# Optimization experiments

Measured on AMD Instinct MI355X. Metric: run time of the kernel, lower is better.

The kernel has to match this reference:

```python
import jax, jax.numpy as jnp
import numpy as np

EMBED_DIM = 1024
NUM_HEADS = 16
HEAD_DIM = EMBED_DIM // NUM_HEADS
FF_DIM = 4096
LN_EPS = 1e-5


def layer_norm(x, scale, bias):
    mu = jnp.mean(x, axis=-1, keepdims=True)
    var = jnp.mean(jnp.square(x - mu), axis=-1, keepdims=True)
    return (x - mu) * jax.lax.rsqrt(var + LN_EPS) * scale + bias


def setup_inputs() -> dict:
    key = jax.random.key(0)
    ks = jax.random.split(key, 9)
    E, F = EMBED_DIM, FF_DIM
    s = lambda d: 1.0 / np.sqrt(d)
    return {
        "x": jax.random.normal(ks[0], (2, 2048, E), dtype=jnp.float32),
        "qkv_w": jax.random.uniform(ks[1], (3 * E, E), jnp.float32, -s(E), s(E)),
        "out_w": jax.random.uniform(ks[2], (E, E), jnp.float32, -s(E), s(E)),
        "ff_up_w": jax.random.uniform(ks[3], (F, E), jnp.float32, -s(E), s(E)),
        "ff_down_w": jax.random.uniform(ks[4], (E, F), jnp.float32, -s(F), s(F)),
        "norm1_scale": jnp.ones((E,), jnp.float32),
        "norm1_bias": jnp.zeros((E,), jnp.float32),
        "norm2_scale": jnp.ones((E,), jnp.float32),
        "norm2_bias": jnp.zeros((E,), jnp.float32),
    }


def reference(x, qkv_w, out_w, ff_up_w, ff_down_w,
              norm1_scale, norm1_bias, norm2_scale, norm2_bias):
    B, S, E = x.shape
    H, D = NUM_HEADS, HEAD_DIM

    # --- attention sublayer ---
    residual = x
    h = layer_norm(x, norm1_scale, norm1_bias)
    qkv = h @ qkv_w.T                               # [B,S,3E]
    qkv = qkv.reshape(B, S, 3, H, D).transpose(2, 0, 3, 1, 4)  # [3,B,H,S,D]
    q, k, v = qkv[0], qkv[1], qkv[2]
    scores = jnp.einsum("bhqd,bhkd->bhqk", q, k) / np.sqrt(D)
    probs = jax.nn.softmax(scores, axis=-1)
    attn = jnp.einsum("bhqk,bhkd->bhqd", probs, v)  # [B,H,S,D]
    attn = attn.transpose(0, 2, 1, 3).reshape(B, S, E)
    x = residual + attn @ out_w.T

    # --- FFN sublayer ---
    residual = x
    h = layer_norm(x, norm2_scale, norm2_bias)
    h = jax.nn.gelu(h @ ff_up_w.T, approximate=False)
    h = h @ ff_down_w.T
    return residual + h
```

## Files before the change

kernel.cpp:

```cpp
#include <hip/hip_runtime.h>

typedef unsigned short u16;
typedef unsigned int u32;
typedef __attribute__((ext_vector_type(8))) short bf16x8;
typedef __attribute__((ext_vector_type(4))) float f32x4;

#define MFMA_BF16(a, b, c) __builtin_amdgcn_mfma_f32_16x16x32_bf16((a), (b), (c), 0, 0, 0)
#define BAR() __builtin_amdgcn_s_barrier()
#define WAITV(n) asm volatile("s_waitcnt vmcnt(" #n ")" ::: "memory")

#if __has_builtin(__builtin_amdgcn_exp2f)
#define EXP2(x) __builtin_amdgcn_exp2f(x)
#else
#define EXP2(x) exp2f(x)
#endif

__device__ __forceinline__ u16 f2bf(float f) {
    u32 u = __builtin_bit_cast(u32, f);
    u32 r = u + 0x7FFFu + ((u >> 16) & 1u);
    return (u16)(r >> 16);
}

__device__ __forceinline__ void gld16(const void* g, void* s) {
    __builtin_amdgcn_global_load_lds(
        (const __attribute__((address_space(1))) unsigned int*)g,
        (__attribute__((address_space(3))) unsigned int*)s, 16, 0, 0);
}

__global__ __launch_bounds__(256) void cvtall_k(const float* __restrict__ w0,
                                                const float* __restrict__ w1,
                                                const float* __restrict__ w2,
                                                const float* __restrict__ w3,
                                                u16* o0, u16* o1, u16* o2, u16* o3) {
    int j = blockIdx.x * 256 + threadIdx.x;
    const float* src; u16* dst;
    if (j < 786432)                       { src = w0; dst = o0; }
    else if ((j -= 786432) < 262144)      { src = w1; dst = o1; }
    else if ((j -= 262144) < 1048576)     { src = w2; dst = o2; }
    else { j -= 1048576;                    src = w3; dst = o3; }
    float4 v = ((const float4*)src)[j];
    ushort4 o;
    o.x = f2bf(v.x); o.y = f2bf(v.y); o.z = f2bf(v.z); o.w = f2bf(v.w);
    ((ushort4*)dst)[j] = o;
}

__global__ __launch_bounds__(256) void ln_k(const float* __restrict__ x,
                                            u16* __restrict__ out,
                                            const float* __restrict__ sc,
                                            const float* __restrict__ bi) {
    const int row = blockIdx.x;
    const int tid = threadIdx.x;
    const float4 v = ((const float4*)(x + (size_t)row * 1024))[tid];
    float s  = v.x + v.y + v.z + v.w;
    float s2 = v.x*v.x + v.y*v.y + v.z*v.z + v.w*v.w;
    #pragma unroll
    for (int m = 32; m; m >>= 1) { s += __shfl_xor(s, m); s2 += __shfl_xor(s2, m); }
    __shared__ float red[8];
    const int w = tid >> 6, l = tid & 63;
    if (l == 0) { red[w] = s; red[4 + w] = s2; }
    __syncthreads();
    s  = red[0] + red[1] + red[2] + red[3];
    s2 = red[4] + red[5] + red[6] + red[7];
    const float mu  = s * (1.0f / 1024.0f);
    const float var = s2 * (1.0f / 1024.0f) - mu * mu;
    const float rs  = rsqrtf(var + 1e-5f);
    const float4 sv = ((const float4*)sc)[tid];
    const float4 bv = ((const float4*)bi)[tid];
    ushort4 o;
    o.x = f2bf((v.x - mu) * rs * sv.x + bv.x);
    o.y = f2bf((v.y - mu) * rs * sv.y + bv.y);
    o.z = f2bf((v.z - mu) * rs * sv.z + bv.z);
    o.w = f2bf((v.w - mu) * rs * sv.w + bv.w);
    ((ushort4*)(out + (size_t)row * 1024))[tid] = o;
}

template<int NT, int EPI>
__global__ __launch_bounds__(512, 1) void gemm256_k(const u16* __restrict__ A,
                                                    const u16* __restrict__ B,
                                                    u16* __restrict__ Cb,
                                                    u16* __restrict__ vtout,
                                                    int M, int N, int K) {
    extern __shared__ u16 L[];
    const int tid = threadIdx.x;
    const int w = tid >> 6, l = tid & 63, g = l >> 4, lc = l & 15;
    const int wr = w >> 2, wc = w & 3;

    const int gx = gridDim.x, gy = gridDim.y;
    const int lin = blockIdx.x + gx * blockIdx.y;
    const int rx = gx >> 2, cy = gy >> 1;
    const int xcd = lin & 7, slot = lin >> 3;
    const int brow = (xcd & 3) * rx + (slot % rx);
    const int bcol = (xcd >> 2) * cy + (slot / rx);
    const int row0 = brow * 256, col0 = bcol * 256;

    const u16* gA = A + (size_t)row0 * K;
    const u16* gB = B + (size_t)col0 * K;
    int srow[4], soct[4];
    #pragma unroll
    for (int p = 0; p < 4; ++p) {
        const int idx = p * 512 + tid;
        srow[p] = idx >> 3;
        soct[p] = (idx & 7) ^ (srow[p] & 7);
    }

#define STG(t, p) do { \
        char* base_ = (char*)L + ((t) & 1) * 65536; \
        gld16(gA + (size_t)srow[p] * K + (size_t)(t) * 64 + soct[p] * 8, \
              base_ + ((p) * 512 + tid) * 16); \
        gld16(gB + (size_t)srow[p] * K + (size_t)(t) * 64 + soct[p] * 8, \
              base_ + 32768 + ((p) * 512 + tid) * 16); \
    } while (0)

    f32x4 acc[8][4] = {};

    STG(0, 0); STG(0, 1); STG(0, 2); STG(0, 3);

    const int ocx = lc & 7;

    for (int t = 0; t < NT; ++t) {
        const bool pf = (t + 1 < NT);
        if (pf) { STG(t + 1, 0); WAITV(2); } else { WAITV(0); }
        BAR();

        const u16* La = L + (t & 1) * 32768;
        const u16* Lb = La + 16384;

        bf16x8 bfr[4][2];
        #pragma unroll
        for (int j = 0; j < 4; ++j)
            #pragma unroll
            for (int kk = 0; kk < 2; ++kk)
                bfr[j][kk] = *(const bf16x8*)
                    &Lb[(wc * 64 + j * 16 + lc) * 64 + (((kk * 4 + g) ^ ocx) * 8)];

        #pragma unroll
        for (int ph = 0; ph < 4; ++ph) {
            if (ph == 2) BAR();
            bf16x8 af[2][2];
            #pragma unroll
            for (int ii = 0; ii < 2; ++ii)
                #pragma unroll
                for (int kk = 0; kk < 2; ++kk)
                    af[ii][kk] = *(const bf16x8*)
                        &La[(wr * 128 + (ph * 2 + ii) * 16 + lc) * 64 +
                            (((kk * 4 + g) ^ ocx) * 8)];
            __builtin_amdgcn_s_setprio(1);
            #pragma unroll
            for (int ii = 0; ii < 2; ++ii)
                #pragma unroll
                for (int j = 0; j < 4; ++j)
                    #pragma unroll
                    for (int kk = 0; kk < 2; ++kk)
                        acc[ph * 2 + ii][j] = MFMA_BF16(af[ii][kk], bfr[j][kk],
                                                        acc[ph * 2 + ii][j]);
            __builtin_amdgcn_s_setprio(0);
            if (pf && ph < 3) STG(t + 1, ph + 1);
        }
    }
#undef STG

    #pragma unroll
    for (int i = 0; i < 8; ++i)
        #pragma unroll
        for (int j = 0; j < 4; ++j) {
            const int rowb = row0 + wr * 128 + i * 16 + g * 4;
            const int col  = col0 + wc * 64 + j * 16 + lc;
            if (EPI == 0 && col >= 2048) {
                u32 lo, hi;
                asm("v_cvt_pk_bf16_f32 %0, %1, %2"
                    : "=v"(lo) : "v"(acc[i][j][0]), "v"(acc[i][j][1]));
                asm("v_cvt_pk_bf16_f32 %0, %1, %2"
                    : "=v"(hi) : "v"(acc[i][j][2]), "v"(acc[i][j][3]));
                const int hd = col - 2048, bb = rowb >> 11, token = rowb & 2047;
                uint2 pk; pk.x = lo; pk.y = hi;
                *(uint2*)(vtout + ((size_t)(bb * 16 + (hd >> 6)) * 64 + (hd & 63)) * 2048
                          + token) = pk;
            } else {
                #pragma unroll
                for (int r = 0; r < 4; ++r) {
                    const size_t off = (size_t)(rowb + r) * N + col;
                    const float v = acc[i][j][r];
                    if (EPI == 0) {
                        const float vv = (col < 1024) ? v * 0.180336880f : v;
                        Cb[off] = f2bf(vv);
                    } else {
                        const float gv = 0.5f * v * (1.0f + erff(v * 0.70710678118f));
                        Cb[off] = f2bf(gv);
                    }
                }
            }
        }
}

template<int NT>
__global__ __launch_bounds__(512, 1) void gemm128w8_k(const u16* __restrict__ A,
                                                      const u16* __restrict__ B,
                                                      float* __restrict__ Cf,
                                                      const float* __restrict__ resid,
                                                      int M, int N, int K) {
    extern __shared__ u16 L[];
    const int tid = threadIdx.x;
    const int w = tid >> 6, l = tid & 63, g = l >> 4, lc = l & 15;
    const int wr = w >> 1, wc = w & 1;
    const int row0 = blockIdx.x * 128, col0 = blockIdx.y * 128;

    const u16* gA = A + (size_t)row0 * K;
    const u16* gB = B + (size_t)col0 * K;
    const int srow = tid >> 3;
    const int soct = (tid & 7) ^ (srow & 7);

#define STG8(t, p) do { \
        const u16* src_ = ((p) < 2) ? gB : gA; \
        const int row_ = (((p) & 1) << 6) + srow; \
        gld16(src_ + (size_t)row_ * K + (size_t)(t) * 64 + soct * 8, \
              (char*)L + ((t) & 1) * 32768 + (p) * 8192 + tid * 16); \
    } while (0)

    f32x4 acc[2][4] = {};

    STG8(0, 0); STG8(0, 1); STG8(0, 2); STG8(0, 3);

    const int ocx = lc & 7;

    for (int t = 0; t < NT; ++t) {
        const bool pf = (t + 1 < NT);
        if (pf) { STG8(t + 1, 0); WAITV(1); } else { WAITV(0); }
        BAR();

        const u16* Lb = L + (t & 1) * 16384;
        const u16* La = Lb + 8192;

        bf16x8 bfr[4][2];
        #pragma unroll
        for (int j = 0; j < 4; ++j)
            #pragma unroll
            for (int kk = 0; kk < 2; ++kk)
                bfr[j][kk] = *(const bf16x8*)
                    &Lb[(wc * 64 + j * 16 + lc) * 64 + (((kk * 4 + g) ^ ocx) * 8)];

        {
            bf16x8 af[2];
            #pragma unroll
            for (int kk = 0; kk < 2; ++kk)
                af[kk] = *(const bf16x8*)
                    &La[(wr * 32 + lc) * 64 + (((kk * 4 + g) ^ ocx) * 8)];
            __builtin_amdgcn_s_setprio(1);
            #pragma unroll
            for (int j = 0; j < 4; ++j)
                #pragma unroll
                for (int kk = 0; kk < 2; ++kk)
                    acc[0][j] = MFMA_BF16(af[kk], bfr[j][kk], acc[0][j]);
            __builtin_amdgcn_s_setprio(0);
        }
        if (pf) { STG8(t + 1, 1); STG8(t + 1, 2); }
        BAR();
        {
            bf16x8 af[2];
            #pragma unroll
            for (int kk = 0; kk < 2; ++kk)
                af[kk] = *(const bf16x8*)
                    &La[(wr * 32 + 16 + lc) * 64 + (((kk * 4 + g) ^ ocx) * 8)];
            __builtin_amdgcn_s_setprio(1);
            #pragma unroll
            for (int j = 0; j < 4; ++j)
                #pragma unroll
                for (int kk = 0; kk < 2; ++kk)
                    acc[1][j] = MFMA_BF16(af[kk], bfr[j][kk], acc[1][j]);
            __builtin_amdgcn_s_setprio(0);
        }
        if (pf) STG8(t + 1, 3);
    }
#undef STG8

    #pragma unroll
    for (int i = 0; i < 2; ++i)
        #pragma unroll
        for (int j = 0; j < 4; ++j)
            #pragma unroll
            for (int r = 0; r < 4; ++r) {
                const int row = row0 + wr * 32 + i * 16 + g * 4 + r;
                const int col = col0 + wc * 64 + j * 16 + lc;
                const size_t off = (size_t)row * N + col;
                Cf[off] = acc[i][j][r] + resid[off];
            }
}

__global__ __launch_bounds__(512) void attn_k(const u16* __restrict__ qkv,
                                              const u16* __restrict__ vt,
                                              u16* __restrict__ ctx) {
    const int bh = blockIdx.x;
    const int qt = blockIdx.y;
    const int b = bh >> 4, h = bh & 15;
    const int tid = threadIdx.x, w = tid >> 6, l = tid & 63, g = l >> 4, lc = l & 15;
    const size_t tok0 = (size_t)b * 2048;

    const u16* Qg  = qkv + (tok0 + qt * 128) * 3072 + h * 64;
    const u16* Kg  = qkv + tok0 * 3072 + 1024 + h * 64;
    const u16* Vtg = vt + (size_t)bh * 64 * 2048;

    __shared__ u16 Ks[2][64 * 64];
    __shared__ u16 Vts[2][64 * 64];
    __shared__ u16 QPs[128 * 64];
    u16* Pw = QPs + w * 1024;

    {
        const int q0r = tid >> 3,         q0c = (tid & 7) ^ (q0r & 7);
        const int q1r = (tid + 512) >> 3, q1c = ((tid + 512) & 7) ^ (q1r & 7);
        gld16(Qg + (size_t)q0r * 3072 + q0c * 8, (char*)QPs + tid * 16);
        gld16(Qg + (size_t)q1r * 3072 + q1c * 8, (char*)QPs + (tid + 512) * 16);
    }
    const int skr = tid >> 3, skc = (tid & 7) ^ (skr & 7);
    const u16* kp = Kg + (size_t)skr * 3072 + skc * 8;
    const u16* vp = Vtg + (size_t)skr * 2048 + skc * 8;
    gld16(kp, (char*)Ks[0] + tid * 16);
    gld16(vp, (char*)Vts[0] + tid * 16);
    kp += 64 * 3072; vp += 64;
    __syncthreads();

    bf16x8 qf[2];
    {
        const int qrow = w * 16 + lc;
        qf[0] = *(const bf16x8*)&QPs[qrow * 64 + ((g       ^ (lc & 7)) * 8)];
        qf[1] = *(const bf16x8*)&QPs[qrow * 64 + (((4 + g) ^ (lc & 7)) * 8)];
    }

    f32x4 oacc[4] = {};
    float mrow = -1e30f, lrow = 0.0f;
    const int hsw = (lc & 7) << 3;

    for (int kt = 0; kt < 32; ++kt) {
        WAITV(0);
        BAR();
        if (kt + 1 < 32) {
            gld16(kp, (char*)Ks[(kt + 1) & 1] + tid * 16);
            gld16(vp, (char*)Vts[(kt + 1) & 1] + tid * 16);
            kp += 64 * 3072; vp += 64;
        }
        const u16* Kc = Ks[kt & 1];
        const u16* Vc = Vts[kt & 1];

        f32x4 sacc[4] = {};
        __builtin_amdgcn_s_setprio(1);
        #pragma unroll
        for (int kk = 0; kk < 2; ++kk)
            #pragma unroll
            for (int nt = 0; nt < 4; ++nt) {
                const int krow = nt * 16 + lc;
                const bf16x8 kb = *(const bf16x8*)
                    &Kc[krow * 64 + (((kk * 4 + g) ^ (lc & 7)) * 8)];
                sacc[nt] = MFMA_BF16(kb, qf[kk], sacc[nt]);
            }
        __builtin_amdgcn_s_setprio(0);

        float mx;
        {
            const float* sv = (const float*)sacc;
            float m = sv[0];
            #pragma unroll
            for (int q = 0; q < 7; ++q) {
                float t;
                asm("v_max3_f32 %0, %1, %2, %3"
                    : "=v"(t) : "v"(m), "v"(sv[2 * q + 1]), "v"(sv[2 * q + 2]));
                m = t;
            }
            mx = fmaxf(m, sv[15]);
        }
        mx = fmaxf(mx, __shfl_xor(mx, 16));
        mx = fmaxf(mx, __shfl_xor(mx, 32));
        const bool ru = __any(mx > mrow + 8.0f);
        float corr = 1.0f;
        if (ru) {
            const float mnew = fmaxf(mrow, mx);
            corr = EXP2(mrow - mnew);
            mrow = mnew;
        }

        float p[4][4];
        float ps = 0.0f;
        #pragma unroll
        for (int nt = 0; nt < 4; ++nt)
            #pragma unroll
            for (int r = 0; r < 4; ++r) {
                const float pv = EXP2(sacc[nt][r] - mrow);
                p[nt][r] = pv;
                ps += pv;
            }
        ps += __shfl_xor(ps, 16);
        ps += __shfl_xor(ps, 32);

        #pragma unroll
        for (int nt = 0; nt < 4; ++nt) {
            uint2 pk;
            asm("v_cvt_pk_bf16_f32 %0, %1, %2" : "=v"(pk.x) : "v"(p[nt][0]), "v"(p[nt][1]));
            asm("v_cvt_pk_bf16_f32 %0, %1, %2" : "=v"(pk.y) : "v"(p[nt][2]), "v"(p[nt][3]));
            *(uint2*)&Pw[lc * 64 + ((nt * 16 + g * 4) ^ hsw)] = pk;
        }

        if (ru) {
            lrow = lrow * corr + ps;
            float cq[4];
            #pragma unroll
            for (int r = 0; r < 4; ++r) cq[r] = __shfl(corr, g * 4 + r);
            #pragma unroll
            for (int nt = 0; nt < 4; ++nt)
                #pragma unroll
                for (int r = 0; r < 4; ++r) oacc[nt][r] *= cq[r];
        } else {
            lrow += ps;
        }

        __builtin_amdgcn_s_setprio(1);
        #pragma unroll
        for (int kk = 0; kk < 2; ++kk) {
            const bf16x8 pa = *(const bf16x8*)
                &Pw[lc * 64 + ((kk * 32 + g * 8) ^ hsw)];
            #pragma unroll
            for (int nt = 0; nt < 4; ++nt) {
                const int vrow = nt * 16 + lc;
                const bf16x8 vb = *(const bf16x8*)
                    &Vc[vrow * 64 + (((kk * 4 + g) ^ (lc & 7)) * 8)];
                oacc[nt] = MFMA_BF16(pa, vb, oacc[nt]);
            }
        }
        __builtin_amdgcn_s_setprio(0);
    }

    float lq[4];
    #pragma unroll
    for (int r = 0; r < 4; ++r) lq[r] = 1.0f / __shfl(lrow, g * 4 + r);
    #pragma unroll
    for (int nt = 0; nt < 4; ++nt)
        #pragma unroll
        for (int r = 0; r < 4; ++r) {
            const float o = oacc[nt][r] * lq[r];
            const size_t token = tok0 + qt * 128 + w * 16 + g * 4 + r;
            ctx[token * 1024 + h * 64 + nt * 16 + lc] = f2bf(o);
        }
}

extern "C" void kernel_launch(void* const* d_in, const int* in_sizes, int n_in,
                              void* d_out, int out_size, void* d_ws, size_t ws_size,
                              hipStream_t stream) {
    const float* x      = (const float*)d_in[0];
    const float* qkv_w  = (const float*)d_in[1];
    const float* out_w  = (const float*)d_in[2];
    const float* up_w   = (const float*)d_in[3];
    const float* down_w = (const float*)d_in[4];
    const float* n1s    = (const float*)d_in[5];
    const float* n1b    = (const float*)d_in[6];
    const float* n2s    = (const float*)d_in[7];
    const float* n2b    = (const float*)d_in[8];
    float* out = (float*)d_out;

    char* ws = (char*)d_ws;
    size_t off = 0;
    auto alloc = [&](size_t bytes) -> void* {
        void* p = ws + off;
        off += (bytes + 255) & ~(size_t)255;
        return p;
    };
    u16*   qkvw_b = (u16*)alloc(3072ull * 1024 * 2);
    u16*   outw_b = (u16*)alloc(1024ull * 1024 * 2);
    u16*   upw_b  = (u16*)alloc(4096ull * 1024 * 2);
    u16*   dnw_b  = (u16*)alloc(1024ull * 4096 * 2);
    u16*   h_b    = (u16*)alloc(4096ull * 1024 * 2);
    u16*   qkv_o  = (u16*)alloc(4096ull * 3072 * 2);
    u16*   ctx    = (u16*)alloc(4096ull * 1024 * 2);
    float* x2     = (float*)alloc(4096ull * 1024 * 4);
    u16*   u      = (u16*)alloc(4096ull * 4096 * 2);
    u16*   vt     = u;

    hipFuncSetAttribute((const void*)&gemm256_k<16, 0>,
                        hipFuncAttributeMaxDynamicSharedMemorySize, 131072);
    hipFuncSetAttribute((const void*)&gemm256_k<16, 2>,
                        hipFuncAttributeMaxDynamicSharedMemorySize, 131072);
    hipFuncSetAttribute((const void*)&gemm128w8_k<16>,
                        hipFuncAttributeMaxDynamicSharedMemorySize, 65536);
    hipFuncSetAttribute((const void*)&gemm128w8_k<64>,
                        hipFuncAttributeMaxDynamicSharedMemorySize, 65536);

    cvtall_k<<<12288, 256, 0, stream>>>(qkv_w, out_w, up_w, down_w,
                                        qkvw_b, outw_b, upw_b, dnw_b);

    ln_k<<<4096, 256, 0, stream>>>(x, h_b, n1s, n1b);
    gemm256_k<16, 0><<<dim3(16, 12), 512, 131072, stream>>>(h_b, qkvw_b, qkv_o, vt,
                                                            4096, 3072, 1024);
    attn_k<<<dim3(32, 16), 512, 0, stream>>>(qkv_o, vt, ctx);
    gemm128w8_k<16><<<dim3(32, 8), 512, 65536, stream>>>(ctx, outw_b, x2, x,
                                                         4096, 1024, 1024);

    ln_k<<<4096, 256, 0, stream>>>(x2, h_b, n2s, n2b);
    gemm256_k<16, 2><<<dim3(16, 16), 512, 131072, stream>>>(h_b, upw_b, u, nullptr,
                                                            4096, 4096, 1024);
    gemm128w8_k<64><<<dim3(32, 8), 512, 65536, stream>>>(u, dnw_b, out, x2,
                                                         4096, 1024, 4096);
}
```

Before: 227.5 us.

## Deepen gemm128w8 LDS pipeline to four stages with single barrier per K step

Converts the 128x128 residual GEMM from a double-buffered, split-phase prefetch into a four-buffer ring that keeps three K tiles in flight via global_load_lds. Each iteration now waits with vmcnt counts, syncs once, issues the prefetch three tiles ahead, then loads both A fragments and runs all MFMAs together. This removes the mid-iteration barrier and hides more memory latency, at the cost of doubling dynamic LDS to 128 KB and holding more fragment registers. It affects the out-projection and FFN down-projection GEMMs, which run 256 blocks on 256 CUs.

```diff
diff --git a/kernel.cpp b/kernel.cpp
--- a/kernel.cpp
+++ b/kernel.cpp
@@ -209,66 +209,56 @@
     const int srow = tid >> 3;
     const int soct = (tid & 7) ^ (srow & 7);
 
-#define STG8(t, p) do { \
-        const u16* src_ = ((p) < 2) ? gB : gA; \
-        const int row_ = (((p) & 1) << 6) + srow; \
-        gld16(src_ + (size_t)row_ * K + (size_t)(t) * 64 + soct * 8, \
-              (char*)L + ((t) & 1) * 32768 + (p) * 8192 + tid * 16); \
+#define STG8(t) do { \
+        char* base_ = (char*)L + ((t) & 3) * 32768; \
+        _Pragma("unroll") \
+        for (int p = 0; p < 4; ++p) { \
+            const u16* src_ = (p < 2) ? gB : gA; \
+            const int row_ = ((p & 1) << 6) + srow; \
+            gld16(src_ + (size_t)row_ * K + (size_t)(t) * 64 + soct * 8, \
+                  base_ + p * 8192 + tid * 16); \
+        } \
     } while (0)
 
     f32x4 acc[2][4] = {};
 
-    STG8(0, 0); STG8(0, 1); STG8(0, 2); STG8(0, 3);
+    STG8(0); STG8(1); STG8(2);
 
     const int ocx = lc & 7;
 
     for (int t = 0; t < NT; ++t) {
-        const bool pf = (t + 1 < NT);
-        if (pf) { STG8(t + 1, 0); WAITV(1); } else { WAITV(0); }
+        if      (t + 2 < NT) WAITV(8);
+        else if (t + 1 < NT) WAITV(4);
+        else                 WAITV(0);
         BAR();
-
-        const u16* Lb = L + (t & 1) * 16384;
+        if (t + 3 < NT) STG8(t + 3);
+
+        const u16* Lb = L + (t & 3) * 16384;
         const u16* La = Lb + 8192;
 
-        bf16x8 bfr[4][2];
+        bf16x8 bfr[4][2], af[2][2];
         #pragma unroll
         for (int j = 0; j < 4; ++j)
             #pragma unroll
             for (int kk = 0; kk < 2; ++kk)
                 bfr[j][kk] = *(const bf16x8*)
                     &Lb[(wc * 64 + j * 16 + lc) * 64 + (((kk * 4 + g) ^ ocx) * 8)];
-
-        {
-            bf16x8 af[2];
+        #pragma unroll
+        for (int ii = 0; ii < 2; ++ii)
             #pragma unroll
             for (int kk = 0; kk < 2; ++kk)
-                af[kk] = *(const bf16x8*)
-                    &La[(wr * 32 + lc) * 64 + (((kk * 4 + g) ^ ocx) * 8)];
-            __builtin_amdgcn_s_setprio(1);
+                af[ii][kk] = *(const bf16x8*)
+                    &La[(wr * 32 + ii * 16 + lc) * 64 + (((kk * 4 + g) ^ ocx) * 8)];
+
+        __builtin_amdgcn_s_setprio(1);
+        #pragma unroll
+        for (int ii = 0; ii < 2; ++ii)
             #pragma unroll
             for (int j = 0; j < 4; ++j)
                 #pragma unroll
                 for (int kk = 0; kk < 2; ++kk)
-                    acc[0][j] = MFMA_BF16(af[kk], bfr[j][kk], acc[0][j]);
-            __builtin_amdgcn_s_setprio(0);
-        }
-        if (pf) { STG8(t + 1, 1); STG8(t + 1, 2); }
-        BAR();
-        {
-            bf16x8 af[2];
-            #pragma unroll
-            for (int kk = 0; kk < 2; ++kk)
-                af[kk] = *(const bf16x8*)
-                    &La[(wr * 32 + 16 + lc) * 64 + (((kk * 4 + g) ^ ocx) * 8)];
-            __builtin_amdgcn_s_setprio(1);
-            #pragma unroll
-            for (int j = 0; j < 4; ++j)
-                #pragma unroll
-                for (int kk = 0; kk < 2; ++kk)
-                    acc[1][j] = MFMA_BF16(af[kk], bfr[j][kk], acc[1][j]);
-            __builtin_amdgcn_s_setprio(0);
-        }
-        if (pf) STG8(t + 1, 3);
+                    acc[ii][j] = MFMA_BF16(af[ii][kk], bfr[j][kk], acc[ii][j]);
+        __builtin_amdgcn_s_setprio(0);
     }
 #undef STG8
 
@@ -475,9 +465,9 @@
     hipFuncSetAttribute((const void*)&gemm256_k<16, 2>,
                         hipFuncAttributeMaxDynamicSharedMemorySize, 131072);
     hipFuncSetAttribute((const void*)&gemm128w8_k<16>,
-                        hipFuncAttributeMaxDynamicSharedMemorySize, 65536);
+                        hipFuncAttributeMaxDynamicSharedMemorySize, 131072);
     hipFuncSetAttribute((const void*)&gemm128w8_k<64>,
-                        hipFuncAttributeMaxDynamicSharedMemorySize, 65536);
+                        hipFuncAttributeMaxDynamicSharedMemorySize, 131072);
 
     cvtall_k<<<12288, 256, 0, stream>>>(qkv_w, out_w, up_w, down_w,
                                         qkvw_b, outw_b, upw_b, dnw_b);
@@ -486,12 +476,12 @@
     gemm256_k<16, 0><<<dim3(16, 12), 512, 131072, stream>>>(h_b, qkvw_b, qkv_o, vt,
                                                             4096, 3072, 1024);
     attn_k<<<dim3(32, 16), 512, 0, stream>>>(qkv_o, vt, ctx);
-    gemm128w8_k<16><<<dim3(32, 8), 512, 65536, stream>>>(ctx, outw_b, x2, x,
-                                                         4096, 1024, 1024);
+    gemm128w8_k<16><<<dim3(32, 8), 512, 131072, stream>>>(ctx, outw_b, x2, x,
+                                                          4096, 1024, 1024);
 
     ln_k<<<4096, 256, 0, stream>>>(x2, h_b, n2s, n2b);
     gemm256_k<16, 2><<<dim3(16, 16), 512, 131072, stream>>>(h_b, upw_b, u, nullptr,
                                                             4096, 4096, 1024);
-    gemm128w8_k<64><<<dim3(32, 8), 512, 65536, stream>>>(u, dnw_b, out, x2,
-                                                         4096, 1024, 4096);
-}
+    gemm128w8_k<64><<<dim3(32, 8), 512, 131072, stream>>>(u, dnw_b, out, x2,
+                                                          4096, 1024, 4096);
+}
```

New measurement: 207.3 us. 8.9% less time.
